# Kernel tuning notes

Measured on AMD Instinct MI355X. Metric: run time of the kernel, lower is better.

## Reference

```python
import jax, jax.numpy as jnp
import numpy as np

N = 100000      # nodes
E = 3200000     # edges
F_IN = 128
HID = 64
NUM_CLASSES = 10
NUM_GRAPHS = 256


def setup_inputs() -> dict:
    key = jax.random.key(0)
    ks = jax.random.split(key, 12)
    x = jax.random.normal(ks[0], (N, F_IN), dtype=jnp.float32)
    edge_index = jax.random.randint(ks[1], (2, E), 0, N, dtype=jnp.int64)
    batch = jnp.sort(jax.random.randint(ks[2], (N,), 0, NUM_GRAPHS, dtype=jnp.int64))
    s = 1.0 / np.sqrt(F_IN)
    W1 = jax.random.uniform(ks[3], (F_IN, HID), jnp.float32, -s, s)
    b1 = jnp.zeros((HID,), jnp.float32)
    s2 = 1.0 / np.sqrt(HID)
    W2 = jax.random.uniform(ks[4], (HID, HID), jnp.float32, -s2, s2)
    b2 = jnp.zeros((HID,), jnp.float32)
    W3 = jax.random.uniform(ks[5], (HID, HID), jnp.float32, -s2, s2)
    b3 = jnp.zeros((HID,), jnp.float32)
    Wc = jax.random.uniform(ks[6], (HID, NUM_CLASSES), jnp.float32, -s2, s2)
    bc = jax.random.uniform(ks[7], (NUM_CLASSES,), jnp.float32, -s2, s2)
    return {"x": x, "edge_index": edge_index, "batch": batch,
            "W1": W1, "b1": b1, "W2": W2, "b2": b2, "W3": W3, "b3": b3,
            "Wc": Wc, "bc": bc}


def _gcn_norm(edge_index, num_nodes):
    # add self-loops, compute symmetric normalization D^-1/2 A_hat D^-1/2
    loop = jnp.arange(num_nodes, dtype=edge_index.dtype)
    src = jnp.concatenate([edge_index[0], loop])
    dst = jnp.concatenate([edge_index[1], loop])
    deg = jax.ops.segment_sum(jnp.ones_like(dst, dtype=jnp.float32), dst,
                              num_segments=num_nodes)
    dinv = jax.lax.rsqrt(deg)  # deg >= 1 due to self-loops
    norm = dinv[src] * dinv[dst]  # [E+N]
    return src, dst, norm


def _gcn_layer(x, W, b, src, dst, norm, num_nodes):
    h = x @ W                              # [N, H] dense transform first (PyG order)
    msg = norm[:, None] * h[src]           # gather + scale
    agg = jax.ops.segment_sum(msg, dst, num_segments=num_nodes)  # scatter-add
    return agg + b


def reference(x, edge_index, batch, W1, b1, W2, b2, W3, b3, Wc, bc):
    num_nodes = x.shape[0]
    src, dst, norm = _gcn_norm(edge_index, num_nodes)
    h = jax.nn.relu(_gcn_layer(x, W1, b1, src, dst, norm, num_nodes))
    h = jax.nn.relu(_gcn_layer(h, W2, b2, src, dst, norm, num_nodes))
    h = jax.nn.relu(_gcn_layer(h, W3, b3, src, dst, norm, num_nodes))
    # global mean pool over graphs
    sums = jax.ops.segment_sum(h, batch, num_segments=NUM_GRAPHS)
    cnt = jax.ops.segment_sum(jnp.ones((num_nodes,), jnp.float32), batch,
                              num_segments=NUM_GRAPHS)
    pooled = sums / jnp.maximum(cnt, 1.0)[:, None]   # [G, HID]
    return pooled @ Wc + bc                          # [G, NUM_CLASSES]
```

## Files before the change

kernel.cpp:

```cpp
#include <hip/hip_runtime.h>


#define NSUB 512
#define MAXNODES 256

typedef __attribute__((ext_vector_type(8))) short bf16x8;
typedef __attribute__((ext_vector_type(4))) float f32x4;

__device__ __forceinline__ unsigned short f2bf(float x) {
  unsigned u = __float_as_uint(x);
  u += 0x7FFFu + ((u >> 16) & 1u);
  return (unsigned short)(u >> 16);
}
__device__ __forceinline__ float bf2f(unsigned short h) {
  return __uint_as_float((unsigned)h << 16);
}
__device__ __forceinline__ float uf(unsigned u) { return __uint_as_float(u); }

__device__ __forceinline__ int idx32(const int* p, long long i, bool wide) {
  return __builtin_nontemporal_load(p + (wide ? 2 * i : i));
}

__global__ __launch_bounds__(1024) void k_part(const void* __restrict__ eiv, int E,
                                               int* __restrict__ flag, int cap2,
                                               int* __restrict__ scur,
                                               unsigned* __restrict__ ebuf2, int N) {
  __shared__ int cnt[NSUB];
  __shared__ int base[NSUB];
  __shared__ int off[NSUB];
  __shared__ int s_any;
  const unsigned* eu = (const unsigned*)eiv;
  const int* ei = (const int*)eiv;
  const int tid = threadIdx.x;
  if (tid == 0) s_any = 0;
  __syncthreads();
  unsigned vv = 0;
  for (int i = tid; i < 8192; i += 1024) vv |= eu[2 * i + 1];
  if (vv) atomicOr(&s_any, 1);
  for (int i = tid; i < NSUB; i += 1024) { cnt[i] = 0; off[i] = 0; }
  __syncthreads();
  const bool wide = (s_any == 0);
  if (blockIdx.x == 0 && tid == 0) *flag = wide ? 1 : 0;
  const int chunk = (E + gridDim.x - 1) / gridDim.x;
  const int c0 = blockIdx.x * chunk;
  const int c1 = (c0 + chunk < E) ? c0 + chunk : E;
  for (int e = c0 + tid; e < c1; e += 1024) {
    const int d = idx32(ei, (long long)E + e, wide);
    const int b = (int)(((long long)d * NSUB) / N);
    atomicAdd(&cnt[b], 1);
  }
  __syncthreads();
  for (int i = tid; i < NSUB; i += 1024) base[i] = atomicAdd(&scur[i], cnt[i]);
  __syncthreads();
  const long long cap = (long long)NSUB * cap2;
  for (int e = c0 + tid; e < c1; e += 1024) {
    const int d = idx32(ei, (long long)E + e, wide);
    const int s = idx32(ei, e, wide);
    const int b = (int)(((long long)d * NSUB) / N);
    const int nlo = (int)(((long long)N * b + NSUB - 1) / NSUB);
    const int o = atomicAdd(&off[b], 1);
    long long pos = (long long)b * cap2 + base[b] + o;
    if (pos >= cap) pos = cap - 1;
    ebuf2[pos] = ((unsigned)(d - nlo) << 24) | (unsigned)s;
  }
}

__global__ __launch_bounds__(512) void k_build(const unsigned* __restrict__ ebuf2,
                                               const int* __restrict__ scur, int cap2,
                                               int* __restrict__ rowptr,
                                               float* __restrict__ dinv,
                                               int* __restrict__ csr, int N) {
  __shared__ int sc[NSUB];
  __shared__ int hist[256];
  __shared__ int pref[256];
  const int s = blockIdx.x;
  const int t = threadIdx.x;
  if (t < NSUB) sc[t] = scur[t];
  __syncthreads();
  for (int off = 1; off < NSUB; off <<= 1) {
    int tv = 0;
    if (t < NSUB && t >= off) tv = sc[t - off];
    __syncthreads();
    if (t < NSUB) sc[t] += tv;
    __syncthreads();
  }
  const int mycnt = scur[s];
  const int sb = sc[s] - mycnt;
  const int total = sc[NSUB - 1];
  int nlo = (int)(((long long)N * s + NSUB - 1) / NSUB);
  int nhi = (int)(((long long)N * (s + 1) + NSUB - 1) / NSUB);
  if (nhi > N) nhi = N;
  const int nn = nhi - nlo;
  if (t < 256) hist[t] = 0;
  __syncthreads();
  const long long e0 = (long long)s * cap2;
  const long long e1 = e0 + mycnt;
  for (long long e = e0 + t; e < e1; e += 512) {
    const unsigned v = __builtin_nontemporal_load(&ebuf2[e]);
    atomicAdd(&hist[v >> 24], 1);
  }
  __syncthreads();
  int h = 0;
  if (t < 256) {
    h = hist[t];
    pref[t] = h;
  }
  __syncthreads();
  for (int off = 1; off < 256; off <<= 1) {
    int tv = 0;
    if (t < 256 && t >= off) tv = pref[t - off];
    __syncthreads();
    if (t < 256) pref[t] += tv;
    __syncthreads();
  }
  if (t < 256) {
    const int cur0 = sb + pref[t] - h;
    if (t < nn) {
      rowptr[nlo + t] = cur0;
      dinv[nlo + t] = rsqrtf((float)(h + 1));
    }
    hist[t] = cur0;
  }
  if (s == NSUB - 1 && t == 0) rowptr[N] = total;
  __syncthreads();
  for (long long e = e0 + t; e < e1; e += 512) {
    const unsigned v = ebuf2[e];
    const int pos = atomicAdd(&hist[v >> 24], 1);
    csr[pos] = (int)(v & 0x00FFFFFFu);
  }
}

template <int K, bool BF16IN>
__global__ __launch_bounds__(256) void k_gemm_mfma(const void* __restrict__ Xv,
                                                   const float* __restrict__ Wg,
                                                   const float* __restrict__ dinv,
                                                   unsigned short* __restrict__ HS,
                                                   int N) {
  __shared__ short Xl[64 * K];
  __shared__ short Wt[64 * K];
  const int t = threadIdx.x;
  const long long r0 = (long long)blockIdx.x * 64;
  const int rows = (int)((N - r0) < 64 ? (N - r0) : 64);

  for (int idx = t; idx < K * 64; idx += 256) {
    const int k = idx >> 6, n = idx & 63;
    Wt[n * K + (((k >> 3) ^ (n & 7)) << 3) + (k & 7)] = (short)f2bf(Wg[idx]);
  }
  const int CH = K / 8;
#pragma unroll
  for (int p = 0; p < K / 32; ++p) {
    const int c = p * 256 + t;
    const int row = c / CH, ch = c % CH;
    const int src = (row < rows) ? row : 0;
    bf16x8 h;
    if constexpr (BF16IN) {
      h = *(const bf16x8*)&((const unsigned short*)Xv)[(r0 + src) * K + ch * 8];
    } else {
      const float* X = (const float*)Xv;
      const float4 v0 = *(const float4*)&X[(r0 + src) * K + ch * 8];
      const float4 v1 = *(const float4*)&X[(r0 + src) * K + ch * 8 + 4];
      h[0] = (short)f2bf(v0.x); h[1] = (short)f2bf(v0.y);
      h[2] = (short)f2bf(v0.z); h[3] = (short)f2bf(v0.w);
      h[4] = (short)f2bf(v1.x); h[5] = (short)f2bf(v1.y);
      h[6] = (short)f2bf(v1.z); h[7] = (short)f2bf(v1.w);
    }
    *(bf16x8*)&Xl[row * K + ((ch ^ (row & 7)) << 3)] = h;
  }
  __syncthreads();

  const int lane = t & 63, w = t >> 6;
  const int lo = lane & 15, hi = lane >> 4;
  const int rowa = w * 16 + lo;

  f32x4 acc[4];
#pragma unroll
  for (int i = 0; i < 4; ++i) acc[i] = (f32x4){0.f, 0.f, 0.f, 0.f};

  bf16x8 a[K / 32];
#pragma unroll
  for (int kk = 0; kk < K / 32; ++kk)
    a[kk] = *(const bf16x8*)&Xl[rowa * K + (((kk * 4 + hi) ^ (rowa & 7)) << 3)];

#pragma unroll
  for (int n0 = 0; n0 < 4; ++n0) {
    const int n = n0 * 16 + lo;
#pragma unroll
    for (int kk = 0; kk < K / 32; ++kk) {
      const bf16x8 b = *(const bf16x8*)&Wt[n * K + (((kk * 4 + hi) ^ (n & 7)) << 3)];
      acc[n0] = __builtin_amdgcn_mfma_f32_16x16x32_bf16(a[kk], b, acc[n0], 0, 0, 0);
    }
  }

  float dv[4];
#pragma unroll
  for (int r = 0; r < 4; ++r) {
    const int rr = w * 16 + hi * 4 + r;
    dv[r] = dinv[r0 + (rr < rows ? rr : 0)];
  }
#pragma unroll
  for (int n0 = 0; n0 < 4; ++n0) {
#pragma unroll
    for (int r = 0; r < 4; ++r) {
      const int rr = w * 16 + hi * 4 + r;
      if (rr < rows)
        HS[(r0 + rr) * 64 + n0 * 16 + lo] = f2bf(dv[r] * acc[n0][r]);
    }
  }
}

__global__ __launch_bounds__(256) void k_agg_gemm(
    const unsigned short* __restrict__ HSin, const int* __restrict__ rowptr,
    const int* __restrict__ csr, const float* __restrict__ dinv,
    const float* __restrict__ bias, const float* __restrict__ Wg,
    unsigned short* __restrict__ HSout, int N) {
  __shared__ short Xl[64 * 64];
  __shared__ short Wt[64 * 64];
  const int t = threadIdx.x;
  const long long r0 = (long long)blockIdx.x * 64;
  const int rows = (int)((N - r0) < 64 ? (N - r0) : 64);
  for (int idx = t; idx < 64 * 64; idx += 256) {
    const int k = idx >> 6, n = idx & 63;
    Wt[n * 64 + (((k >> 3) ^ (n & 7)) << 3) + (k & 7)] = (short)f2bf(Wg[idx]);
  }
  if (rows < 64) {
    for (int i = t; i < 64 * 64; i += 256) Xl[i] = 0;
  }
  __syncthreads();

  const int lane = t & 63;
  const int wid = t >> 6;
  const int c4 = lane & 15;
  const int q = lane >> 4;
  const float bb0 = bias[4 * c4 + 0], bb1 = bias[4 * c4 + 1];
  const float bb2 = bias[4 * c4 + 2], bb3 = bias[4 * c4 + 3];
  const uint2* __restrict__ H8 = (const uint2*)HSin;
  const unsigned M = 0xffff0000u;
  for (int i = 0; i < 16; ++i) {
    const int row = wid * 16 + i;
    if (row >= rows) break;
    const int node = (int)(r0 + row);
    const int s0 = rowptr[node], s1 = rowptr[node + 1];
    float a0 = 0.f, a1 = 0.f, a2 = 0.f, a3 = 0.f;
    float c0 = 0.f, c1 = 0.f, c2 = 0.f, c3 = 0.f;
    if (q == 0) {
      const uint2 u = H8[(long long)node * 16 + c4];
      a0 += uf(u.x << 16); a1 += uf(u.x & M);
      a2 += uf(u.y << 16); a3 += uf(u.y & M);
    }
    for (int base = s0; base < s1; base += 64) {
      int m = s1 - base;
      if (m > 64) m = 64;
      const int idx = (base + lane < s1) ? csr[base + lane] : 0;
      const int ng = m >> 2;
      int g = 0;
      for (; g + 2 <= ng; g += 2) {
        const int e0 = __shfl(idx, 4 * g + q, 64);
        const int e1 = __shfl(idx, 4 * g + 4 + q, 64);
        const uint2 u0 = H8[(long long)e0 * 16 + c4];
        const uint2 u1 = H8[(long long)e1 * 16 + c4];
        a0 += uf(u0.x << 16); a1 += uf(u0.x & M);
        a2 += uf(u0.y << 16); a3 += uf(u0.y & M);
        c0 += uf(u1.x << 16); c1 += uf(u1.x & M);
        c2 += uf(u1.y << 16); c3 += uf(u1.y & M);
      }
      for (; g < ng; ++g) {
        const int e0 = __shfl(idx, 4 * g + q, 64);
        const uint2 u0 = H8[(long long)e0 * 16 + c4];
        a0 += uf(u0.x << 16); a1 += uf(u0.x & M);
        a2 += uf(u0.y << 16); a3 += uf(u0.y & M);
      }
      const int rm = m & 3;
      if (rm) {
        const int e = __shfl(idx, (m & ~3) + (q < rm ? q : 0), 64);
        if (q < rm) {
          const uint2 u = H8[(long long)e * 16 + c4];
          a0 += uf(u.x << 16); a1 += uf(u.x & M);
          a2 += uf(u.y << 16); a3 += uf(u.y & M);
        }
      }
    }
    a0 += c0; a1 += c1; a2 += c2; a3 += c3;
    a0 += __shfl_xor(a0, 16, 64); a0 += __shfl_xor(a0, 32, 64);
    a1 += __shfl_xor(a1, 16, 64); a1 += __shfl_xor(a1, 32, 64);
    a2 += __shfl_xor(a2, 16, 64); a2 += __shfl_xor(a2, 32, 64);
    a3 += __shfl_xor(a3, 16, 64); a3 += __shfl_xor(a3, 32, 64);
    if (q == 0) {
      const float dv = dinv[node];
      const unsigned short o0 = f2bf(fmaxf(fmaf(dv, a0, bb0), 0.f));
      const unsigned short o1 = f2bf(fmaxf(fmaf(dv, a1, bb1), 0.f));
      const unsigned short o2 = f2bf(fmaxf(fmaf(dv, a2, bb2), 0.f));
      const unsigned short o3 = f2bf(fmaxf(fmaf(dv, a3, bb3), 0.f));
      uint2 o;
      o.x = (unsigned)o0 | ((unsigned)o1 << 16);
      o.y = (unsigned)o2 | ((unsigned)o3 << 16);
      const int ch = c4 >> 1;
      *(uint2*)&Xl[row * 64 + ((ch ^ (row & 7)) << 3) + (c4 & 1) * 4] = o;
    }
  }
  __syncthreads();

  const int lo = lane & 15, hi = lane >> 4;
  const int rowa = wid * 16 + lo;
  f32x4 acc[4];
#pragma unroll
  for (int i = 0; i < 4; ++i) acc[i] = (f32x4){0.f, 0.f, 0.f, 0.f};
  bf16x8 a[2];
#pragma unroll
  for (int kk = 0; kk < 2; ++kk)
    a[kk] = *(const bf16x8*)&Xl[rowa * 64 + (((kk * 4 + hi) ^ (rowa & 7)) << 3)];
#pragma unroll
  for (int n0 = 0; n0 < 4; ++n0) {
    const int n = n0 * 16 + lo;
#pragma unroll
    for (int kk = 0; kk < 2; ++kk) {
      const bf16x8 b = *(const bf16x8*)&Wt[n * 64 + (((kk * 4 + hi) ^ (n & 7)) << 3)];
      acc[n0] = __builtin_amdgcn_mfma_f32_16x16x32_bf16(a[kk], b, acc[n0], 0, 0, 0);
    }
  }
  float dvv[4];
#pragma unroll
  for (int r = 0; r < 4; ++r) {
    const int rr = wid * 16 + hi * 4 + r;
    dvv[r] = dinv[r0 + (rr < rows ? rr : 0)];
  }
#pragma unroll
  for (int n0 = 0; n0 < 4; ++n0) {
#pragma unroll
    for (int r = 0; r < 4; ++r) {
      const int rr = wid * 16 + hi * 4 + r;
      if (rr < rows)
        HSout[(r0 + rr) * 64 + n0 * 16 + lo] = f2bf(dvv[r] * acc[n0][r]);
    }
  }
}

__global__ void k_agg(const unsigned short* __restrict__ HS, const int* __restrict__ rowptr,
                      const int* __restrict__ csr, const float* __restrict__ dinv,
                      const float* __restrict__ bias, unsigned* __restrict__ OUT, int N) {
  const int lane = threadIdx.x & 63;
  const int wid = threadIdx.x >> 6;
  const int wpb = blockDim.x >> 6;
  const int c4 = lane & 15;
  const int q = lane >> 4;
  const float b0 = bias[4 * c4 + 0], b1 = bias[4 * c4 + 1];
  const float b2 = bias[4 * c4 + 2], b3 = bias[4 * c4 + 3];
  const uint2* __restrict__ H8 = (const uint2*)HS;
  uint2* __restrict__ O8 = (uint2*)OUT;
  const unsigned M = 0xffff0000u;
  for (int node = blockIdx.x * wpb + wid; node < N; node += wpb * gridDim.x) {
    const int s0 = rowptr[node], s1 = rowptr[node + 1];
    float a0 = 0.f, a1 = 0.f, a2 = 0.f, a3 = 0.f;
    float c0 = 0.f, c1 = 0.f, c2 = 0.f, c3 = 0.f;
    if (q == 0) {
      const uint2 u = H8[(long long)node * 16 + c4];
      a0 += uf(u.x << 16); a1 += uf(u.x & M);
      a2 += uf(u.y << 16); a3 += uf(u.y & M);
    }
    for (int base = s0; base < s1; base += 64) {
      int m = s1 - base;
      if (m > 64) m = 64;
      const int idx = (base + lane < s1) ? csr[base + lane] : 0;
      const int ng = m >> 2;
      int g = 0;
      for (; g + 2 <= ng; g += 2) {
        const int e0 = __shfl(idx, 4 * g + q, 64);
        const int e1 = __shfl(idx, 4 * g + 4 + q, 64);
        const uint2 u0 = H8[(long long)e0 * 16 + c4];
        const uint2 u1 = H8[(long long)e1 * 16 + c4];
        a0 += uf(u0.x << 16); a1 += uf(u0.x & M);
        a2 += uf(u0.y << 16); a3 += uf(u0.y & M);
        c0 += uf(u1.x << 16); c1 += uf(u1.x & M);
        c2 += uf(u1.y << 16); c3 += uf(u1.y & M);
      }
      for (; g < ng; ++g) {
        const int e0 = __shfl(idx, 4 * g + q, 64);
        const uint2 u0 = H8[(long long)e0 * 16 + c4];
        a0 += uf(u0.x << 16); a1 += uf(u0.x & M);
        a2 += uf(u0.y << 16); a3 += uf(u0.y & M);
      }
      const int rm = m & 3;
      if (rm) {
        const int e = __shfl(idx, (m & ~3) + (q < rm ? q : 0), 64);
        if (q < rm) {
          const uint2 u = H8[(long long)e * 16 + c4];
          a0 += uf(u.x << 16); a1 += uf(u.x & M);
          a2 += uf(u.y << 16); a3 += uf(u.y & M);
        }
      }
    }
    a0 += c0; a1 += c1; a2 += c2; a3 += c3;
    a0 += __shfl_xor(a0, 16, 64); a0 += __shfl_xor(a0, 32, 64);
    a1 += __shfl_xor(a1, 16, 64); a1 += __shfl_xor(a1, 32, 64);
    a2 += __shfl_xor(a2, 16, 64); a2 += __shfl_xor(a2, 32, 64);
    a3 += __shfl_xor(a3, 16, 64); a3 += __shfl_xor(a3, 32, 64);
    if (q == 0) {
      const float dv = dinv[node];
      const unsigned short o0 = f2bf(fmaxf(fmaf(dv, a0, b0), 0.f));
      const unsigned short o1 = f2bf(fmaxf(fmaf(dv, a1, b1), 0.f));
      const unsigned short o2 = f2bf(fmaxf(fmaf(dv, a2, b2), 0.f));
      const unsigned short o3 = f2bf(fmaxf(fmaf(dv, a3, b3), 0.f));
      uint2 o;
      o.x = (unsigned)o0 | ((unsigned)o1 << 16);
      o.y = (unsigned)o2 | ((unsigned)o3 << 16);
      O8[(long long)node * 16 + c4] = o;
    }
  }
}

__global__ void k_poolcls(const unsigned short* __restrict__ H,
                          const void* __restrict__ batch, const int* __restrict__ flag,
                          const float* __restrict__ Wc, const float* __restrict__ bc,
                          float* __restrict__ out, int N) {
  __shared__ int se[2];
  __shared__ float red[4][64];
  __shared__ float pl[64];
  bool wide = (*flag != 0);
  int g = blockIdx.x;
  if (threadIdx.x < 2) {
    int target = g + threadIdx.x;
    int lo = 0, hi = N;
    while (lo < hi) {
      int mid = (lo + hi) >> 1;
      long long v = wide ? ((const long long*)batch)[mid] : (long long)((const int*)batch)[mid];
      if (v < target) lo = mid + 1; else hi = mid;
    }
    se[threadIdx.x] = lo;
  }
  __syncthreads();
  int s = se[0], e = se[1];
  int lane = threadIdx.x & 63, wid = threadIdx.x >> 6;
  float acc = 0.f;
  for (int r = s + wid; r < e; r += 4) acc += bf2f(H[(long long)r * 64 + lane]);
  red[wid][lane] = acc;
  __syncthreads();
  if (wid == 0) {
    float v = red[0][lane] + red[1][lane] + red[2][lane] + red[3][lane];
    float cnt = (float)(e - s);
    pl[lane] = v / fmaxf(cnt, 1.f);
  }
  __syncthreads();
  if (threadIdx.x < 10) {
    float a = bc[threadIdx.x];
#pragma unroll
    for (int h = 0; h < 64; ++h) a += pl[h] * Wc[h * 10 + threadIdx.x];
    out[g * 10 + threadIdx.x] = a;
  }
}

extern "C" void kernel_launch(void* const* d_in, const int* in_sizes, int n_in,
                              void* d_out, int out_size, void* d_ws, size_t ws_size,
                              hipStream_t stream) {
  const float* x = (const float*)d_in[0];
  const void* ei = d_in[1];
  const void* batch = d_in[2];
  const float* W1 = (const float*)d_in[3];
  const float* b1 = (const float*)d_in[4];
  const float* W2 = (const float*)d_in[5];
  const float* b2 = (const float*)d_in[6];
  const float* W3 = (const float*)d_in[7];
  const float* b3 = (const float*)d_in[8];
  const float* Wc = (const float*)d_in[9];
  const float* bc = (const float*)d_in[10];
  float* out = (float*)d_out;

  const int N = in_sizes[0] / 128;
  const int E = in_sizes[1] / 2;
  const int G = out_size / 10;
  const int cap2 = E / NSUB + E / NSUB / 8 + 64;

  char* W = (char*)d_ws;
  size_t off = 0;
  auto take = [&](size_t b) -> void* {
    void* p = W + off;
    off += (b + 255) & ~(size_t)255;
    return p;
  };
  int* flag = (int*)take(4);
  int* rowptr = (int*)take((size_t)4 * (N + 1));
  int* scur = (int*)take((size_t)4 * NSUB);
  float* dinv = (float*)take((size_t)4 * N);
  int* csr = (int*)take((size_t)4 * E);
  unsigned short* hsA = (unsigned short*)take((size_t)2 * N * 64);
  unsigned short* hsB = (unsigned short*)take((size_t)2 * N * 64);
  unsigned* ebuf2 = (unsigned*)take((size_t)4 * NSUB * cap2);
  (void)ws_size;

  hipMemsetAsync(scur, 0, (size_t)4 * NSUB, stream);

  k_part<<<512, 1024, 0, stream>>>(ei, E, flag, cap2, scur, ebuf2, N);
  k_build<<<NSUB, 512, 0, stream>>>(ebuf2, scur, cap2, rowptr, dinv, csr, N);

  const int TILES = (N + 63) / 64;
  k_gemm_mfma<128, false><<<TILES, 256, 0, stream>>>(x, W1, dinv, hsA, N);
  k_agg_gemm<<<TILES, 256, 0, stream>>>(hsA, rowptr, csr, dinv, b1, W2, hsB, N);
  k_agg_gemm<<<TILES, 256, 0, stream>>>(hsB, rowptr, csr, dinv, b2, W3, hsA, N);
  k_agg<<<4096, 256, 0, stream>>>(hsA, rowptr, csr, dinv, b3, (unsigned*)hsB, N);

  k_poolcls<<<G, 256, 0, stream>>>(hsB, batch, flag, Wc, bc, out, N);
}
```

Baseline: 330.1 us.

## Fuse last-layer aggregation with mean pooling and stash edges in registers during CSR build

The final GCN aggregation kernel now accumulates ReLU outputs per graph in registers and atomically adds partial sums into a pooled buffer. This removes the write of the last hidden layer and the pooling kernel's reread of it, and leaves a small classifier kernel. Separately, k_build keeps up to 16 edge entries per thread in registers between the histogram pass and the scatter pass, so that pass does not reload them from global memory. The cost is float atomics whose order varies from run to run, a fixed 64-node tiling in place of a grid-stride loop, and higher register pressure in k_build.

```diff
diff --git a/kernel.cpp b/kernel.cpp
--- a/kernel.cpp
+++ b/kernel.cpp
@@ -65,6 +65,7 @@
   }
 }
 
+#define STASHJ 16
 __global__ __launch_bounds__(512) void k_build(const unsigned* __restrict__ ebuf2,
                                                const int* __restrict__ scur, int cap2,
                                                int* __restrict__ rowptr,
@@ -95,7 +96,17 @@
   __syncthreads();
   const long long e0 = (long long)s * cap2;
   const long long e1 = e0 + mycnt;
-  for (long long e = e0 + t; e < e1; e += 512) {
+  unsigned stash[STASHJ];
+#pragma unroll
+  for (int j = 0; j < STASHJ; ++j) {
+    const long long e = e0 + t + (long long)j * 512;
+    if (e < e1) {
+      const unsigned v = __builtin_nontemporal_load(&ebuf2[e]);
+      stash[j] = v;
+      atomicAdd(&hist[v >> 24], 1);
+    }
+  }
+  for (long long e = e0 + t + (long long)STASHJ * 512; e < e1; e += 512) {
     const unsigned v = __builtin_nontemporal_load(&ebuf2[e]);
     atomicAdd(&hist[v >> 24], 1);
   }
@@ -123,7 +134,16 @@
   }
   if (s == NSUB - 1 && t == 0) rowptr[N] = total;
   __syncthreads();
-  for (long long e = e0 + t; e < e1; e += 512) {
+#pragma unroll
+  for (int j = 0; j < STASHJ; ++j) {
+    const long long e = e0 + t + (long long)j * 512;
+    if (e < e1) {
+      const unsigned v = stash[j];
+      const int pos = atomicAdd(&hist[v >> 24], 1);
+      csr[pos] = (int)(v & 0x00FFFFFFu);
+    }
+  }
+  for (long long e = e0 + t + (long long)STASHJ * 512; e < e1; e += 512) {
     const unsigned v = ebuf2[e];
     const int pos = atomicAdd(&hist[v >> 24], 1);
     csr[pos] = (int)(v & 0x00FFFFFFu);
@@ -334,20 +354,31 @@
   }
 }
 
-__global__ void k_agg(const unsigned short* __restrict__ HS, const int* __restrict__ rowptr,
-                      const int* __restrict__ csr, const float* __restrict__ dinv,
-                      const float* __restrict__ bias, unsigned* __restrict__ OUT, int N) {
-  const int lane = threadIdx.x & 63;
-  const int wid = threadIdx.x >> 6;
-  const int wpb = blockDim.x >> 6;
+__global__ __launch_bounds__(256) void k_agg_pool(
+    const unsigned short* __restrict__ HS, const int* __restrict__ rowptr,
+    const int* __restrict__ csr, const float* __restrict__ dinv,
+    const float* __restrict__ bias, const void* __restrict__ batch,
+    const int* __restrict__ flag, float* __restrict__ pooled, int N) {
+  const int t = threadIdx.x;
+  const long long r0 = (long long)blockIdx.x * 64;
+  const int rows = (int)((N - r0) < 64 ? (N - r0) : 64);
+  const int lane = t & 63;
+  const int wid = t >> 6;
   const int c4 = lane & 15;
   const int q = lane >> 4;
-  const float b0 = bias[4 * c4 + 0], b1 = bias[4 * c4 + 1];
-  const float b2 = bias[4 * c4 + 2], b3 = bias[4 * c4 + 3];
+  const bool wideB = (*flag != 0);
+  const int* bi = (const int*)batch;
+  const float bb0 = bias[4 * c4 + 0], bb1 = bias[4 * c4 + 1];
+  const float bb2 = bias[4 * c4 + 2], bb3 = bias[4 * c4 + 3];
   const uint2* __restrict__ H8 = (const uint2*)HS;
-  uint2* __restrict__ O8 = (uint2*)OUT;
   const unsigned M = 0xffff0000u;
-  for (int node = blockIdx.x * wpb + wid; node < N; node += wpb * gridDim.x) {
+  float ps0 = 0.f, ps1 = 0.f, ps2 = 0.f, ps3 = 0.f;
+  int gcur = -1;
+  for (int i = 0; i < 16; ++i) {
+    const int row = wid * 16 + i;
+    if (row >= rows) break;
+    const int node = (int)(r0 + row);
+    const int g = wideB ? (int)((const long long*)batch)[node] : bi[node];
     const int s0 = rowptr[node], s1 = rowptr[node + 1];
     float a0 = 0.f, a1 = 0.f, a2 = 0.f, a3 = 0.f;
     float c0 = 0.f, c1 = 0.f, c2 = 0.f, c3 = 0.f;
@@ -361,10 +392,10 @@
       if (m > 64) m = 64;
       const int idx = (base + lane < s1) ? csr[base + lane] : 0;
       const int ng = m >> 2;
-      int g = 0;
-      for (; g + 2 <= ng; g += 2) {
-        const int e0 = __shfl(idx, 4 * g + q, 64);
-        const int e1 = __shfl(idx, 4 * g + 4 + q, 64);
+      int gg = 0;
+      for (; gg + 2 <= ng; gg += 2) {
+        const int e0 = __shfl(idx, 4 * gg + q, 64);
+        const int e1 = __shfl(idx, 4 * gg + 4 + q, 64);
         const uint2 u0 = H8[(long long)e0 * 16 + c4];
         const uint2 u1 = H8[(long long)e1 * 16 + c4];
         a0 += uf(u0.x << 16); a1 += uf(u0.x & M);
@@ -372,8 +403,8 @@
         c0 += uf(u1.x << 16); c1 += uf(u1.x & M);
         c2 += uf(u1.y << 16); c3 += uf(u1.y & M);
       }
-      for (; g < ng; ++g) {
-        const int e0 = __shfl(idx, 4 * g + q, 64);
+      for (; gg < ng; ++gg) {
+        const int e0 = __shfl(idx, 4 * gg + q, 64);
         const uint2 u0 = H8[(long long)e0 * 16 + c4];
         a0 += uf(u0.x << 16); a1 += uf(u0.x & M);
         a2 += uf(u0.y << 16); a3 += uf(u0.y & M);
@@ -393,29 +424,42 @@
     a1 += __shfl_xor(a1, 16, 64); a1 += __shfl_xor(a1, 32, 64);
     a2 += __shfl_xor(a2, 16, 64); a2 += __shfl_xor(a2, 32, 64);
     a3 += __shfl_xor(a3, 16, 64); a3 += __shfl_xor(a3, 32, 64);
+    if (g != gcur) {
+      if (gcur >= 0 && q == 0) {
+        atomicAdd(&pooled[gcur * 64 + 4 * c4 + 0], ps0);
+        atomicAdd(&pooled[gcur * 64 + 4 * c4 + 1], ps1);
+        atomicAdd(&pooled[gcur * 64 + 4 * c4 + 2], ps2);
+        atomicAdd(&pooled[gcur * 64 + 4 * c4 + 3], ps3);
+      }
+      ps0 = ps1 = ps2 = ps3 = 0.f;
+      gcur = g;
+    }
     if (q == 0) {
       const float dv = dinv[node];
-      const unsigned short o0 = f2bf(fmaxf(fmaf(dv, a0, b0), 0.f));
-      const unsigned short o1 = f2bf(fmaxf(fmaf(dv, a1, b1), 0.f));
-      const unsigned short o2 = f2bf(fmaxf(fmaf(dv, a2, b2), 0.f));
-      const unsigned short o3 = f2bf(fmaxf(fmaf(dv, a3, b3), 0.f));
-      uint2 o;
-      o.x = (unsigned)o0 | ((unsigned)o1 << 16);
-      o.y = (unsigned)o2 | ((unsigned)o3 << 16);
-      O8[(long long)node * 16 + c4] = o;
-    }
-  }
-}
-
-__global__ void k_poolcls(const unsigned short* __restrict__ H,
-                          const void* __restrict__ batch, const int* __restrict__ flag,
-                          const float* __restrict__ Wc, const float* __restrict__ bc,
-                          float* __restrict__ out, int N) {
+      ps0 += fmaxf(fmaf(dv, a0, bb0), 0.f);
+      ps1 += fmaxf(fmaf(dv, a1, bb1), 0.f);
+      ps2 += fmaxf(fmaf(dv, a2, bb2), 0.f);
+      ps3 += fmaxf(fmaf(dv, a3, bb3), 0.f);
+    }
+  }
+  if (gcur >= 0 && q == 0) {
+    atomicAdd(&pooled[gcur * 64 + 4 * c4 + 0], ps0);
+    atomicAdd(&pooled[gcur * 64 + 4 * c4 + 1], ps1);
+    atomicAdd(&pooled[gcur * 64 + 4 * c4 + 2], ps2);
+    atomicAdd(&pooled[gcur * 64 + 4 * c4 + 3], ps3);
+  }
+}
+
+__global__ __launch_bounds__(64) void k_cls(const float* __restrict__ pooled,
+                                            const void* __restrict__ batch,
+                                            const int* __restrict__ flag,
+                                            const float* __restrict__ Wc,
+                                            const float* __restrict__ bc,
+                                            float* __restrict__ out, int N) {
   __shared__ int se[2];
-  __shared__ float red[4][64];
   __shared__ float pl[64];
-  bool wide = (*flag != 0);
-  int g = blockIdx.x;
+  const bool wide = (*flag != 0);
+  const int g = blockIdx.x;
   if (threadIdx.x < 2) {
     int target = g + threadIdx.x;
     int lo = 0, hi = N;
@@ -427,17 +471,8 @@
     se[threadIdx.x] = lo;
   }
   __syncthreads();
-  int s = se[0], e = se[1];
-  int lane = threadIdx.x & 63, wid = threadIdx.x >> 6;
-  float acc = 0.f;
-  for (int r = s + wid; r < e; r += 4) acc += bf2f(H[(long long)r * 64 + lane]);
-  red[wid][lane] = acc;
-  __syncthreads();
-  if (wid == 0) {
-    float v = red[0][lane] + red[1][lane] + red[2][lane] + red[3][lane];
-    float cnt = (float)(e - s);
-    pl[lane] = v / fmaxf(cnt, 1.f);
-  }
+  const float cnt = (float)(se[1] - se[0]);
+  pl[threadIdx.x] = pooled[g * 64 + threadIdx.x] / fmaxf(cnt, 1.f);
   __syncthreads();
   if (threadIdx.x < 10) {
     float a = bc[threadIdx.x];
@@ -478,6 +513,7 @@
   int* flag = (int*)take(4);
   int* rowptr = (int*)take((size_t)4 * (N + 1));
   int* scur = (int*)take((size_t)4 * NSUB);
+  float* pooled = (float*)take((size_t)4 * G * 64);
   float* dinv = (float*)take((size_t)4 * N);
   int* csr = (int*)take((size_t)4 * E);
   unsigned short* hsA = (unsigned short*)take((size_t)2 * N * 64);
@@ -485,7 +521,7 @@
   unsigned* ebuf2 = (unsigned*)take((size_t)4 * NSUB * cap2);
   (void)ws_size;
 
-  hipMemsetAsync(scur, 0, (size_t)4 * NSUB, stream);
+  hipMemsetAsync(scur, 0, (size_t)2048 + (size_t)4 * G * 64, stream);
 
   k_part<<<512, 1024, 0, stream>>>(ei, E, flag, cap2, scur, ebuf2, N);
   k_build<<<NSUB, 512, 0, stream>>>(ebuf2, scur, cap2, rowptr, dinv, csr, N);
@@ -494,7 +530,7 @@
   k_gemm_mfma<128, false><<<TILES, 256, 0, stream>>>(x, W1, dinv, hsA, N);
   k_agg_gemm<<<TILES, 256, 0, stream>>>(hsA, rowptr, csr, dinv, b1, W2, hsB, N);
   k_agg_gemm<<<TILES, 256, 0, stream>>>(hsB, rowptr, csr, dinv, b2, W3, hsA, N);
-  k_agg<<<4096, 256, 0, stream>>>(hsA, rowptr, csr, dinv, b3, (unsigned*)hsB, N);
-
-  k_poolcls<<<G, 256, 0, stream>>>(hsB, batch, flag, Wc, bc, out, N);
-}
+  k_agg_pool<<<TILES, 256, 0, stream>>>(hsA, rowptr, csr, dinv, b3, batch, flag,
+                                        pooled, N);
+  k_cls<<<G, 64, 0, stream>>>(pooled, batch, flag, Wc, bc, out, N);
+}
```

After: 309.1 us. -6.4%, faster.
